# Performance work log

Hardware: AMD Instinct MI355X
Metric: run time of the kernel (lower is better)

Reference implementation:

```python
import jax, jax.numpy as jnp
import numpy as np

B, XDIM, S = 32768, 32, 16
N_COMBINE = XDIM - 2  # 30 combines with out_channels=S (block0 + middle blocks)


def setup_inputs() -> dict:
    key = jax.random.key(0)
    k1, k2, k3, k4 = jax.random.split(key, 4)
    x = jax.random.randint(k1, (B, XDIM), 0, 2, dtype=jnp.int32)  # binary data
    leaf_logits = jax.random.normal(k2, (XDIM, S), dtype=jnp.float32)  # Bernoulli leaf logits per var
    sum_weights = jax.random.normal(k3, (N_COMBINE, S * S, S), dtype=jnp.float32)
    sum_weights_last = jax.random.normal(k4, (S * S, 1), dtype=jnp.float32)
    return {"x": x, "leaf_logits": leaf_logits, "sum_weights": sum_weights,
            "sum_weights_last": sum_weights_last}


def _combine(a, b, W):
    # a, b: [B, S] log-likelihoods; W: [S*S, OC] raw sum weights.
    # CrossProduct in log domain: out[:, i*S + j] = a[:, i] + b[:, j]
    cross = (a[:, :, None] + b[:, None, :]).reshape(a.shape[0], S * S)  # [B, S*S]
    logw = jax.nn.log_softmax(W, axis=0)  # normalize over in_channels
    # Sum node in log domain: logsumexp over input channels
    return jax.nn.logsumexp(cross[:, :, None] + logw[None, :, :], axis=1)  # [B, OC]


def reference(x, leaf_logits, sum_weights, sum_weights_last):
    xf = x.astype(jnp.float32)[:, :, None]  # [B, XDIM, 1]
    # Bernoulli leaf log-prob: x*log(sigmoid(l)) + (1-x)*log(1-sigmoid(l))
    lp = (xf * jax.nn.log_sigmoid(leaf_logits)[None]
          + (1.0 - xf) * jax.nn.log_sigmoid(-leaf_logits)[None])  # [B, XDIM, S]

    # block 0: combine leaves of vars 0 and 1
    curr = _combine(lp[:, 0], lp[:, 1], sum_weights[0])  # [B, S]

    # middle blocks: fold in vars 2 .. XDIM-2
    mid_leaves = jnp.swapaxes(lp[:, 2:XDIM - 1], 0, 1)  # [XDIM-3, B, S]

    def step(c, inp):
        leaf, W = inp
        return _combine(c, leaf, W), None

    curr, _ = jax.lax.scan(step, curr, (mid_leaves, sum_weights[1:]))

    # final block: fold in last var with out_channels=1 root sum
    out = _combine(curr, lp[:, XDIM - 1], sum_weights_last)  # [B, 1]
    return out[:, None, :]  # [B, 1, 1] to match torch output shape
```

## Files before the change

### kernel.cpp

```cpp
#include <hip/hip_runtime.h>

using uint = unsigned int;

#define DW_LO    0
#define DW_HIb   7616
#define DW_FT    15232
#define DW_DELTA 15360
#define DW_BASE  15392
#define DW_EB0   15396
#define DW_TOT   15616

template<int K>
__device__ __forceinline__ int roti(int x) {
    return __builtin_amdgcn_update_dpp(0, x, 0x120 | K, 0xF, 0xF, true);
}
template<int K>
__device__ __forceinline__ float rotf(float x) {
    return __builtin_bit_cast(float, roti<K>(__builtin_bit_cast(int, x)));
}
__device__ __forceinline__ float rowmax16(float d) {
    d = fmaxf(d, rotf<1>(d)); d = fmaxf(d, rotf<2>(d));
    d = fmaxf(d, rotf<4>(d)); d = fmaxf(d, rotf<8>(d));
    return d;
}
__device__ __forceinline__ float rowsum16(float d) {
    d += rotf<1>(d); d += rotf<2>(d); d += rotf<4>(d); d += rotf<8>(d);
    return d;
}
__device__ __forceinline__ float logsig(float z) {
    return fminf(z, 0.f) - log1pf(__expf(-fabsf(z)));
}
__device__ __forceinline__ uint bfpack(float a, float b) {
    uint ua = __builtin_bit_cast(uint, a);
    uint ub = __builtin_bit_cast(uint, b);
    ua = (ua + 0x7fffu + ((ua >> 16) & 1u)) >> 16;
    ub = ((ub + 0x7fffu + ((ub >> 16) & 1u)) >> 16) << 16;
    return ua | ub;
}
__device__ __forceinline__ float blo(uint u) { return __builtin_bit_cast(float, u << 16); }
__device__ __forceinline__ float bhi(uint u) { return __builtin_bit_cast(float, u & 0xffff0000u); }
__device__ __forceinline__ unsigned spread16(unsigned u) {
    u = (u | (u << 8)) & 0x00FF00FFu;
    u = (u | (u << 4)) & 0x0F0F0F0Fu;
    u = (u | (u << 2)) & 0x33333333u;
    u = (u | (u << 1)) & 0x55555555u;
    return u;
}

__global__ __launch_bounds__(512) void prep(const float* __restrict__ sw,
                                            const float* __restrict__ swl,
                                            const float* __restrict__ ll,
                                            float* __restrict__ ws) {
    __shared__ __align__(16) float WFs[2048];
    __shared__ float pm[1024];
    __shared__ float CM[64], CS[64];
    __shared__ float ebs[128];
    __shared__ float Ts[1024];
    __shared__ float Ms[4096];
    __shared__ float BMs[64];
    __shared__ float WLs[32];
    __shared__ float pml[16], psl[16];
    __shared__ float CMl, CSl;

    const int tid = threadIdx.x;
    const int p = blockIdx.x;
    const int oc = tid & 15;
    const int i0 = (tid >> 4) & 15;

    int s1 = roti<1>(oc) & 15,   s2 = roti<2>(oc) & 15,   s3 = roti<3>(oc) & 15;
    int s4 = roti<4>(oc) & 15,   s5 = roti<5>(oc) & 15,   s6 = roti<6>(oc) & 15;
    int s7 = roti<7>(oc) & 15,   s8 = roti<8>(oc) & 15,   s9 = roti<9>(oc) & 15;
    int s10 = roti<10>(oc) & 15, s11 = roti<11>(oc) & 15, s12 = roti<12>(oc) & 15;
    int s13 = roti<13>(oc) & 15, s14 = roti<14>(oc) & 15, s15 = roti<15>(oc) & 15;
    int sidx[16] = {oc, s1, s2, s3, s4, s5, s6, s7, s8, s9, s10, s11, s12, s13, s14, s15};

    if (p < 7) {
        if (tid < 128) {
            int cc = tid >> 5, bb = (tid >> 4) & 1, var = 4 * p + 1 + cc;
            float l = ll[var * 16 + oc];
            float lp = bb ? logsig(l) : logsig(-l);
            ebs[tid] = __expf(lp - rowmax16(lp));
        }
        const float* Wb = sw + p * 4 * 4096;
        const int cc0 = tid >> 8, cc1 = cc0 + 2;
        float w0[16], w1[16];
        float m0 = -1e30f, m1 = -1e30f;
        #pragma unroll
        for (int j = 0; j < 16; ++j) {
            w0[j] = Wb[cc0 * 4096 + (i0 * 16 + j) * 16 + oc];
            w1[j] = Wb[cc1 * 4096 + (i0 * 16 + j) * 16 + oc];
            m0 = fmaxf(m0, w0[j]); m1 = fmaxf(m1, w1[j]);
        }
        pm[cc0 * 256 + oc * 16 + i0] = m0;
        pm[cc1 * 256 + oc * 16 + i0] = m1;
        __syncthreads();
        if (tid < 64) {
            const float* q = pm + (tid >> 4) * 256 + (tid & 15) * 16;
            float m = q[0];
            #pragma unroll
            for (int r = 1; r < 16; ++r) m = fmaxf(m, q[r]);
            CM[tid] = m;
        }
        __syncthreads();
        float cm0 = CM[cc0 * 16 + oc], cm1 = CM[cc1 * 16 + oc];
        float e0[16], e1[16];
        float su0 = 0.f, su1 = 0.f;
        #pragma unroll
        for (int j = 0; j < 16; ++j) {
            e0[j] = __expf(w0[j] - cm0); su0 += e0[j];
            e1[j] = __expf(w1[j] - cm1); su1 += e1[j];
        }
        pm[cc0 * 256 + oc * 16 + i0] = su0;
        pm[cc1 * 256 + oc * 16 + i0] = su1;
        __syncthreads();
        if (tid < 64) {
            const float* q = pm + (tid >> 4) * 256 + (tid & 15) * 16;
            float s = 0.f;
            #pragma unroll
            for (int r = 0; r < 16; ++r) s += q[r];
            CS[tid] = 1.0f / s;
        }
        __syncthreads();
        {
            float inv0 = CS[cc0 * 16 + oc], inv1 = CS[cc1 * 16 + oc];
            float a00 = 0.f, a01 = 0.f, a10 = 0.f, a11 = 0.f;
            #pragma unroll
            for (int j = 0; j < 16; ++j) {
                a00 += ebs[(cc0 * 2 + 0) * 16 + j] * e0[j];
                a01 += ebs[(cc0 * 2 + 1) * 16 + j] * e0[j];
                a10 += ebs[(cc1 * 2 + 0) * 16 + j] * e1[j];
                a11 += ebs[(cc1 * 2 + 1) * 16 + j] * e1[j];
            }
            WFs[(cc0 * 2 + 0) * 256 + i0 * 16 + oc] = a00 * inv0;
            WFs[(cc0 * 2 + 1) * 256 + i0 * 16 + oc] = a01 * inv0;
            WFs[(cc1 * 2 + 0) * 256 + i0 * 16 + oc] = a10 * inv1;
            WFs[(cc1 * 2 + 1) * 256 + i0 * 16 + oc] = a11 * inv1;
        }
        __syncthreads();

        float t1[4], t2[4];
        if (tid < 256) {
            float wf0[2], wf2[2];
            wf0[0] = WFs[0 * 256 + i0 * 16 + oc];
            wf0[1] = WFs[1 * 256 + i0 * 16 + oc];
            wf2[0] = WFs[4 * 256 + i0 * 16 + oc];
            wf2[1] = WFs[5 * 256 + i0 * 16 + oc];
            {
                float w10 = WFs[2 * 256 + oc * 16 + oc], w11 = WFs[3 * 256 + oc * 16 + oc];
                float w30 = WFs[6 * 256 + oc * 16 + oc], w31 = WFs[7 * 256 + oc * 16 + oc];
                t1[0] = wf0[0] * w10; t1[1] = wf0[1] * w10;
                t1[2] = wf0[0] * w11; t1[3] = wf0[1] * w11;
                t2[0] = wf2[0] * w30; t2[1] = wf2[1] * w30;
                t2[2] = wf2[0] * w31; t2[3] = wf2[1] * w31;
            }
            #define QSTEP(T) { \
                float r0 = rotf<T>(wf0[0]), r1 = rotf<T>(wf0[1]); \
                float w10 = WFs[2 * 256 + sidx[T] * 16 + oc], w11 = WFs[3 * 256 + sidx[T] * 16 + oc]; \
                t1[0] = fmaf(r0, w10, t1[0]); t1[1] = fmaf(r1, w10, t1[1]); \
                t1[2] = fmaf(r0, w11, t1[2]); t1[3] = fmaf(r1, w11, t1[3]); \
                float q0 = rotf<T>(wf2[0]), q1 = rotf<T>(wf2[1]); \
                float w30 = WFs[6 * 256 + sidx[T] * 16 + oc], w31 = WFs[7 * 256 + sidx[T] * 16 + oc]; \
                t2[0] = fmaf(q0, w30, t2[0]); t2[1] = fmaf(q1, w30, t2[1]); \
                t2[2] = fmaf(q0, w31, t2[2]); t2[3] = fmaf(q1, w31, t2[3]); }
            QSTEP(1) QSTEP(2) QSTEP(3) QSTEP(4) QSTEP(5) QSTEP(6) QSTEP(7) QSTEP(8)
            QSTEP(9) QSTEP(10) QSTEP(11) QSTEP(12) QSTEP(13) QSTEP(14) QSTEP(15)
            #undef QSTEP
            #pragma unroll
            for (int b = 0; b < 4; ++b) Ts[b * 256 + i0 * 16 + oc] = t2[b];
        }
        __syncthreads();
        if (tid < 256) {
            float M[16];
            {
                float c0 = Ts[0 * 256 + oc * 16 + oc], c1 = Ts[1 * 256 + oc * 16 + oc];
                float c2 = Ts[2 * 256 + oc * 16 + oc], c3 = Ts[3 * 256 + oc * 16 + oc];
                #pragma unroll
                for (int b12 = 0; b12 < 4; ++b12) {
                    M[b12 + 0]  = t1[b12] * c0;
                    M[b12 + 4]  = t1[b12] * c1;
                    M[b12 + 8]  = t1[b12] * c2;
                    M[b12 + 12] = t1[b12] * c3;
                }
            }
            #define MSTEP(T) { \
                float c0 = Ts[0 * 256 + sidx[T] * 16 + oc], c1 = Ts[1 * 256 + sidx[T] * 16 + oc]; \
                float c2 = Ts[2 * 256 + sidx[T] * 16 + oc], c3 = Ts[3 * 256 + sidx[T] * 16 + oc]; \
                float r0 = rotf<T>(t1[0]), r1 = rotf<T>(t1[1]), r2 = rotf<T>(t1[2]), r3 = rotf<T>(t1[3]); \
                M[0]  = fmaf(r0, c0, M[0]);  M[1]  = fmaf(r1, c0, M[1]); \
                M[2]  = fmaf(r2, c0, M[2]);  M[3]  = fmaf(r3, c0, M[3]); \
                M[4]  = fmaf(r0, c1, M[4]);  M[5]  = fmaf(r1, c1, M[5]); \
                M[6]  = fmaf(r2, c1, M[6]);  M[7]  = fmaf(r3, c1, M[7]); \
                M[8]  = fmaf(r0, c2, M[8]);  M[9]  = fmaf(r1, c2, M[9]); \
                M[10] = fmaf(r2, c2, M[10]); M[11] = fmaf(r3, c2, M[11]); \
                M[12] = fmaf(r0, c3, M[12]); M[13] = fmaf(r1, c3, M[13]); \
                M[14] = fmaf(r2, c3, M[14]); M[15] = fmaf(r3, c3, M[15]); }
            MSTEP(1) MSTEP(2) MSTEP(3) MSTEP(4) MSTEP(5) MSTEP(6) MSTEP(7) MSTEP(8)
            MSTEP(9) MSTEP(10) MSTEP(11) MSTEP(12) MSTEP(13) MSTEP(14) MSTEP(15)
            #undef MSTEP
            #pragma unroll
            for (int v = 0; v < 16; ++v) Ms[v * 256 + i0 * 16 + oc] = M[v];
        }
        __syncthreads();
        if (tid < 256) {
            int v = i0, ocx = oc;
            const float* m = Ms + v * 256;
            float x0 = m[ocx * 16 + ocx];
            float x1 = m[s1 * 16 + ocx],   x2 = m[s2 * 16 + ocx],   x3 = m[s3 * 16 + ocx];
            float x4 = m[s4 * 16 + ocx],   x5 = m[s5 * 16 + ocx],   x6 = m[s6 * 16 + ocx];
            float x7 = m[s7 * 16 + ocx],   x8 = m[s8 * 16 + ocx],   x9 = m[s9 * 16 + ocx];
            float x10 = m[s10 * 16 + ocx], x11 = m[s11 * 16 + ocx], x12 = m[s12 * 16 + ocx];
            float x13 = m[s13 * 16 + ocx], x14 = m[s14 * 16 + ocx], x15 = m[s15 * 16 + ocx];
            uint4 lo4, hi4;
            lo4.x = bfpack(x0, x1);   lo4.y = bfpack(x2, x3);
            lo4.z = bfpack(x4, x5);   lo4.w = bfpack(x6, x7);
            hi4.x = bfpack(x8, x9);   hi4.y = bfpack(x10, x11);
            hi4.z = bfpack(x12, x13); hi4.w = bfpack(x14, x15);
            uint* wsu = (uint*)ws;
            int dw = p * 1088 + v * 68 + ocx * 4;
            *(uint4*)(wsu + dw) = lo4;
            *(uint4*)(wsu + DW_HIb + dw) = hi4;
        }
    } else {
        if (tid < 96) {
            int cb = tid >> 4, bb = cb & 1;
            int var = (cb < 4) ? (29 + (cb >> 1)) : 31;
            float l = ll[var * 16 + oc];
            float lp = bb ? logsig(l) : logsig(-l);
            ebs[tid] = __expf(lp - rowmax16(lp));
        }
        const int cc = tid >> 8;
        float w[16]; float m0 = -1e30f;
        #pragma unroll
        for (int j = 0; j < 16; ++j) {
            w[j] = sw[(28 + cc) * 4096 + (i0 * 16 + j) * 16 + oc];
            m0 = fmaxf(m0, w[j]);
        }
        pm[cc * 256 + oc * 16 + i0] = m0;
        float vL = 0.f;
        if (tid >= 256) {
            int u = tid - 256;
            vL = swl[u];
            float pmx = rowmax16(vL);
            if ((u & 15) == 0) pml[u >> 4] = pmx;
        }
        __syncthreads();
        if (tid < 32) {
            const float* q = pm + (tid >> 4) * 256 + (tid & 15) * 16;
            float m = q[0];
            #pragma unroll
            for (int r = 1; r < 16; ++r) m = fmaxf(m, q[r]);
            CM[tid] = m;
        }
        if (tid == 256) {
            float m = pml[0];
            #pragma unroll
            for (int r = 1; r < 16; ++r) m = fmaxf(m, pml[r]);
            CMl = m;
        }
        __syncthreads();
        float cm = CM[cc * 16 + oc];
        float e[16]; float su = 0.f;
        #pragma unroll
        for (int j = 0; j < 16; ++j) { e[j] = __expf(w[j] - cm); su += e[j]; }
        pm[cc * 256 + oc * 16 + i0] = su;
        float eL = 0.f;
        if (tid >= 256) {
            int u = tid - 256;
            eL = __expf(vL - CMl);
            float ps = rowsum16(eL);
            if ((u & 15) == 0) psl[u >> 4] = ps;
        }
        __syncthreads();
        if (tid < 32) {
            const float* q = pm + (tid >> 4) * 256 + (tid & 15) * 16;
            float s = 0.f;
            #pragma unroll
            for (int r = 0; r < 16; ++r) s += q[r];
            CS[tid] = 1.0f / s;
        }
        if (tid == 256) {
            float s = 0.f;
            #pragma unroll
            for (int r = 0; r < 16; ++r) s += psl[r];
            CSl = 1.0f / s;
        }
        __syncthreads();
        {
            float inv = CS[cc * 16 + oc];
            float a0 = 0.f, a1 = 0.f;
            #pragma unroll
            for (int j = 0; j < 16; ++j) {
                a0 += ebs[(cc * 2 + 0) * 16 + j] * e[j];
                a1 += ebs[(cc * 2 + 1) * 16 + j] * e[j];
            }
            WFs[(cc * 2 + 0) * 256 + i0 * 16 + oc] = a0 * inv;
            WFs[(cc * 2 + 1) * 256 + i0 * 16 + oc] = a1 * inv;
        }
        if (tid >= 256) {
            int u = tid - 256, iw = u >> 4;
            float t0 = rowsum16(ebs[64 + oc] * eL);
            float t1 = rowsum16(ebs[80 + oc] * eL);
            if (oc == 0) { WLs[iw] = t0 * CSl; WLs[16 + iw] = t1 * CSl; }
        }
        if (tid < 64) {
            int var = tid >> 1, bb = tid & 1;
            float mm_ = -1e30f;
            #pragma unroll
            for (int j = 0; j < 16; ++j) {
                float l = ll[var * 16 + j];
                mm_ = fmaxf(mm_, bb ? logsig(l) : logsig(-l));
            }
            BMs[tid] = mm_;
        }
        if (tid >= 64 && tid < 96) {
            int u = tid - 64, bb = u >> 4, j = u & 15;
            float mm_ = -1e30f;
            #pragma unroll
            for (int jj = 0; jj < 16; ++jj) {
                float l = ll[jj];
                mm_ = fmaxf(mm_, bb ? logsig(l) : logsig(-l));
            }
            float l = ll[j];
            ws[DW_EB0 + u] = __expf((bb ? logsig(l) : logsig(-l)) - mm_);
        }
        __syncthreads();
        if (tid < 256) {
            float wf28[2];
            wf28[0] = WFs[0 * 256 + i0 * 16 + oc];
            wf28[1] = WFs[1 * 256 + i0 * 16 + oc];
            float t01[4];
            {
                float w0_ = WFs[2 * 256 + oc * 16 + oc], w1_ = WFs[3 * 256 + oc * 16 + oc];
                t01[0] = wf28[0] * w0_; t01[1] = wf28[1] * w0_;
                t01[2] = wf28[0] * w1_; t01[3] = wf28[1] * w1_;
            }
            #define FSTEP(T) { \
                float r0 = rotf<T>(wf28[0]), r1 = rotf<T>(wf28[1]); \
                float w0_ = WFs[2 * 256 + sidx[T] * 16 + oc], w1_ = WFs[3 * 256 + sidx[T] * 16 + oc]; \
                t01[0] = fmaf(r0, w0_, t01[0]); t01[1] = fmaf(r1, w0_, t01[1]); \
                t01[2] = fmaf(r0, w1_, t01[2]); t01[3] = fmaf(r1, w1_, t01[3]); }
            FSTEP(1) FSTEP(2) FSTEP(3) FSTEP(4) FSTEP(5) FSTEP(6) FSTEP(7) FSTEP(8)
            FSTEP(9) FSTEP(10) FSTEP(11) FSTEP(12) FSTEP(13) FSTEP(14) FSTEP(15)
            #undef FSTEP
            float wl0 = WLs[oc], wl1 = WLs[16 + oc];
            #pragma unroll
            for (int v = 0; v < 8; ++v) {
                float f = rowsum16(t01[v & 3] * ((v >> 2) ? wl1 : wl0));
                if (oc == 0) ws[DW_FT + v * 16 + i0] = f;
            }
        }
        if (tid < 32) ws[DW_DELTA + tid] = BMs[2 * tid + 1] - BMs[2 * tid];
        if (tid < 64) {
            float vb = (tid < 32) ? BMs[2 * tid] : 0.f;
            #pragma unroll
            for (int off = 32; off >= 1; off >>= 1) vb += __shfl_xor(vb, off);
            if (tid == 0) ws[DW_BASE] = vb;
        }
    }
}

__device__ __forceinline__ float quadstep(const uint* sPT, float acc, int dw) {
    uint4 wl4 = *(const uint4*)(sPT + dw);
    uint4 wh4 = *(const uint4*)(sPT + DW_HIb + dw);
    float d0 = acc * blo(wl4.x);
    d0 = fmaf(rotf<1>(acc), bhi(wl4.x), d0);
    d0 = fmaf(rotf<2>(acc), blo(wl4.y), d0);
    d0 = fmaf(rotf<3>(acc), bhi(wl4.y), d0);
    d0 = fmaf(rotf<4>(acc), blo(wl4.z), d0);
    d0 = fmaf(rotf<5>(acc), bhi(wl4.z), d0);
    d0 = fmaf(rotf<6>(acc), blo(wl4.w), d0);
    d0 = fmaf(rotf<7>(acc), bhi(wl4.w), d0);
    float d1 = rotf<8>(acc) * blo(wh4.x);
    d1 = fmaf(rotf<9>(acc),  bhi(wh4.x), d1);
    d1 = fmaf(rotf<10>(acc), blo(wh4.y), d1);
    d1 = fmaf(rotf<11>(acc), bhi(wh4.y), d1);
    d1 = fmaf(rotf<12>(acc), blo(wh4.z), d1);
    d1 = fmaf(rotf<13>(acc), bhi(wh4.z), d1);
    d1 = fmaf(rotf<14>(acc), blo(wh4.w), d1);
    d1 = fmaf(rotf<15>(acc), bhi(wh4.w), d1);
    return d0 + d1;
}

__global__ __launch_bounds__(512, 4) void spn_main(const int* __restrict__ x,
                                                   const float* __restrict__ ws,
                                                   float* __restrict__ out) {
    __shared__ __align__(16) float sL[DW_TOT];
    const int tid = threadIdx.x;
    const int g = tid >> 4, oc = tid & 15;
    const int b0 = blockIdx.x * 64 + g;
    const int b1 = b0 + 32;

    int2 xa = *(const int2*)(x + b0 * 32 + 2 * oc);
    int2 xb = *(const int2*)(x + b1 * 32 + 2 * oc);
    unsigned long long ma0 = __ballot(xa.x & 1);
    unsigned long long ma1 = __ballot(xa.y & 1);
    unsigned long long mb0 = __ballot(xb.x & 1);
    unsigned long long mb1 = __ballot(xb.y & 1);
    const int gw = g & 3;
    unsigned bitsA = spread16((unsigned)(ma0 >> (gw * 16)) & 0xffffu)
                   | (spread16((unsigned)(ma1 >> (gw * 16)) & 0xffffu) << 1);
    unsigned bitsB = spread16((unsigned)(mb0 >> (gw * 16)) & 0xffffu)
                   | (spread16((unsigned)(mb1 >> (gw * 16)) & 0xffffu) << 1);

    for (int k = tid; k < DW_TOT / 4; k += 512)
        ((float4*)sL)[k] = ((const float4*)ws)[k];
    __syncthreads();

    float2 dl = *(const float2*)(sL + DW_DELTA + 2 * oc);
    float pa = ((xa.x & 1) ? dl.x : 0.f) + ((xa.y & 1) ? dl.y : 0.f);
    float pb = ((xb.x & 1) ? dl.x : 0.f) + ((xb.y & 1) ? dl.y : 0.f);
    float base = sL[DW_BASE];
    float LA = base + rowsum16(pa);
    float LB = base + rowsum16(pb);

    float accA = sL[DW_EB0 + (bitsA & 1) * 16 + oc];
    float accB = sL[DW_EB0 + (bitsB & 1) * 16 + oc];
    const uint* sPT = (const uint*)sL;
    const int ocd = oc * 4;

    #pragma unroll
    for (int p = 0; p < 7; ++p) {
        int dwA = p * 1088 + (int)((bitsA >> (4 * p + 1)) & 15) * 68 + ocd;
        int dwB = p * 1088 + (int)((bitsB >> (4 * p + 1)) & 15) * 68 + ocd;
        float dA = quadstep(sPT, accA, dwA);
        float dB = quadstep(sPT, accB, dwB);
        if (p & 1) {
            float mA = rowmax16(dA), mB = rowmax16(dB);
            accA = dA * __builtin_amdgcn_rcpf(mA);
            accB = dB * __builtin_amdgcn_rcpf(mB);
            LA += __logf(mA);
            LB += __logf(mB);
        } else {
            accA = dA; accB = dB;
        }
    }

    float tsA = rowsum16(accA * sL[DW_FT + ((bitsA >> 29) & 7) * 16 + oc]);
    float tsB = rowsum16(accB * sL[DW_FT + ((bitsB >> 29) & 7) * 16 + oc]);
    if (oc == 0) {
        out[b0] = LA + __logf(tsA);
        out[b1] = LB + __logf(tsB);
    }
}

extern "C" void kernel_launch(void* const* d_in, const int* in_sizes, int n_in,
                              void* d_out, int out_size, void* d_ws, size_t ws_size,
                              hipStream_t stream) {
    const int*   x   = (const int*)d_in[0];
    const float* ll  = (const float*)d_in[1];
    const float* sw  = (const float*)d_in[2];
    const float* swl = (const float*)d_in[3];
    float* out = (float*)d_out;
    float* ws  = (float*)d_ws;

    hipLaunchKernelGGL(prep,     dim3(8),   dim3(512), 0, stream, sw, swl, ll, ws);
    hipLaunchKernelGGL(spn_main, dim3(512), dim3(512), 0, stream, x, ws, out);
}
```

Baseline: 22.24 us.

## Fuse prep into main kernel with atomic role assignment and spin-wait

Merges the weight-preprocessing kernel into the main kernel. The first eight blocks to arrive, chosen by an atomic ticket, compute the preprocessed tables into workspace and signal a global counter. All blocks spin until that counter reaches eight, then load the tables into shared memory. This removes the second kernel launch and its launch gap. In exchange it adds a memset, a global spin barrier and the risk of stalls if the preprocessing blocks are delayed.

```diff
diff --git a/kernel.cpp b/kernel.cpp
--- a/kernel.cpp
+++ b/kernel.cpp
@@ -9,6 +9,21 @@
 #define DW_BASE  15392
 #define DW_EB0   15396
 #define DW_TOT   15616
+#define DW_CTL   15616
+
+#define oWF   0
+#define oPM   2048
+#define oCM   3072
+#define oCS   3136
+#define oEB   3200
+#define oT    3328
+#define oMM   4352
+#define oBM   8448
+#define oWL   8512
+#define oPML  8544
+#define oPSL  8560
+#define oCML  8576
+#define oCSL  8577
 
 template<int K>
 __device__ __forceinline__ int roti(int x) {
@@ -45,318 +60,6 @@
     u = (u | (u << 2)) & 0x33333333u;
     u = (u | (u << 1)) & 0x55555555u;
     return u;
-}
-
-__global__ __launch_bounds__(512) void prep(const float* __restrict__ sw,
-                                            const float* __restrict__ swl,
-                                            const float* __restrict__ ll,
-                                            float* __restrict__ ws) {
-    __shared__ __align__(16) float WFs[2048];
-    __shared__ float pm[1024];
-    __shared__ float CM[64], CS[64];
-    __shared__ float ebs[128];
-    __shared__ float Ts[1024];
-    __shared__ float Ms[4096];
-    __shared__ float BMs[64];
-    __shared__ float WLs[32];
-    __shared__ float pml[16], psl[16];
-    __shared__ float CMl, CSl;
-
-    const int tid = threadIdx.x;
-    const int p = blockIdx.x;
-    const int oc = tid & 15;
-    const int i0 = (tid >> 4) & 15;
-
-    int s1 = roti<1>(oc) & 15,   s2 = roti<2>(oc) & 15,   s3 = roti<3>(oc) & 15;
-    int s4 = roti<4>(oc) & 15,   s5 = roti<5>(oc) & 15,   s6 = roti<6>(oc) & 15;
-    int s7 = roti<7>(oc) & 15,   s8 = roti<8>(oc) & 15,   s9 = roti<9>(oc) & 15;
-    int s10 = roti<10>(oc) & 15, s11 = roti<11>(oc) & 15, s12 = roti<12>(oc) & 15;
-    int s13 = roti<13>(oc) & 15, s14 = roti<14>(oc) & 15, s15 = roti<15>(oc) & 15;
-    int sidx[16] = {oc, s1, s2, s3, s4, s5, s6, s7, s8, s9, s10, s11, s12, s13, s14, s15};
-
-    if (p < 7) {
-        if (tid < 128) {
-            int cc = tid >> 5, bb = (tid >> 4) & 1, var = 4 * p + 1 + cc;
-            float l = ll[var * 16 + oc];
-            float lp = bb ? logsig(l) : logsig(-l);
-            ebs[tid] = __expf(lp - rowmax16(lp));
-        }
-        const float* Wb = sw + p * 4 * 4096;
-        const int cc0 = tid >> 8, cc1 = cc0 + 2;
-        float w0[16], w1[16];
-        float m0 = -1e30f, m1 = -1e30f;
-        #pragma unroll
-        for (int j = 0; j < 16; ++j) {
-            w0[j] = Wb[cc0 * 4096 + (i0 * 16 + j) * 16 + oc];
-            w1[j] = Wb[cc1 * 4096 + (i0 * 16 + j) * 16 + oc];
-            m0 = fmaxf(m0, w0[j]); m1 = fmaxf(m1, w1[j]);
-        }
-        pm[cc0 * 256 + oc * 16 + i0] = m0;
-        pm[cc1 * 256 + oc * 16 + i0] = m1;
-        __syncthreads();
-        if (tid < 64) {
-            const float* q = pm + (tid >> 4) * 256 + (tid & 15) * 16;
-            float m = q[0];
-            #pragma unroll
-            for (int r = 1; r < 16; ++r) m = fmaxf(m, q[r]);
-            CM[tid] = m;
-        }
-        __syncthreads();
-        float cm0 = CM[cc0 * 16 + oc], cm1 = CM[cc1 * 16 + oc];
-        float e0[16], e1[16];
-        float su0 = 0.f, su1 = 0.f;
-        #pragma unroll
-        for (int j = 0; j < 16; ++j) {
-            e0[j] = __expf(w0[j] - cm0); su0 += e0[j];
-            e1[j] = __expf(w1[j] - cm1); su1 += e1[j];
-        }
-        pm[cc0 * 256 + oc * 16 + i0] = su0;
-        pm[cc1 * 256 + oc * 16 + i0] = su1;
-        __syncthreads();
-        if (tid < 64) {
-            const float* q = pm + (tid >> 4) * 256 + (tid & 15) * 16;
-            float s = 0.f;
-            #pragma unroll
-            for (int r = 0; r < 16; ++r) s += q[r];
-            CS[tid] = 1.0f / s;
-        }
-        __syncthreads();
-        {
-            float inv0 = CS[cc0 * 16 + oc], inv1 = CS[cc1 * 16 + oc];
-            float a00 = 0.f, a01 = 0.f, a10 = 0.f, a11 = 0.f;
-            #pragma unroll
-            for (int j = 0; j < 16; ++j) {
-                a00 += ebs[(cc0 * 2 + 0) * 16 + j] * e0[j];
-                a01 += ebs[(cc0 * 2 + 1) * 16 + j] * e0[j];
-                a10 += ebs[(cc1 * 2 + 0) * 16 + j] * e1[j];
-                a11 += ebs[(cc1 * 2 + 1) * 16 + j] * e1[j];
-            }
-            WFs[(cc0 * 2 + 0) * 256 + i0 * 16 + oc] = a00 * inv0;
-            WFs[(cc0 * 2 + 1) * 256 + i0 * 16 + oc] = a01 * inv0;
-            WFs[(cc1 * 2 + 0) * 256 + i0 * 16 + oc] = a10 * inv1;
-            WFs[(cc1 * 2 + 1) * 256 + i0 * 16 + oc] = a11 * inv1;
-        }
-        __syncthreads();
-
-        float t1[4], t2[4];
-        if (tid < 256) {
-            float wf0[2], wf2[2];
-            wf0[0] = WFs[0 * 256 + i0 * 16 + oc];
-            wf0[1] = WFs[1 * 256 + i0 * 16 + oc];
-            wf2[0] = WFs[4 * 256 + i0 * 16 + oc];
-            wf2[1] = WFs[5 * 256 + i0 * 16 + oc];
-            {
-                float w10 = WFs[2 * 256 + oc * 16 + oc], w11 = WFs[3 * 256 + oc * 16 + oc];
-                float w30 = WFs[6 * 256 + oc * 16 + oc], w31 = WFs[7 * 256 + oc * 16 + oc];
-                t1[0] = wf0[0] * w10; t1[1] = wf0[1] * w10;
-                t1[2] = wf0[0] * w11; t1[3] = wf0[1] * w11;
-                t2[0] = wf2[0] * w30; t2[1] = wf2[1] * w30;
-                t2[2] = wf2[0] * w31; t2[3] = wf2[1] * w31;
-            }
-            #define QSTEP(T) { \
-                float r0 = rotf<T>(wf0[0]), r1 = rotf<T>(wf0[1]); \
-                float w10 = WFs[2 * 256 + sidx[T] * 16 + oc], w11 = WFs[3 * 256 + sidx[T] * 16 + oc]; \
-                t1[0] = fmaf(r0, w10, t1[0]); t1[1] = fmaf(r1, w10, t1[1]); \
-                t1[2] = fmaf(r0, w11, t1[2]); t1[3] = fmaf(r1, w11, t1[3]); \
-                float q0 = rotf<T>(wf2[0]), q1 = rotf<T>(wf2[1]); \
-                float w30 = WFs[6 * 256 + sidx[T] * 16 + oc], w31 = WFs[7 * 256 + sidx[T] * 16 + oc]; \
-                t2[0] = fmaf(q0, w30, t2[0]); t2[1] = fmaf(q1, w30, t2[1]); \
-                t2[2] = fmaf(q0, w31, t2[2]); t2[3] = fmaf(q1, w31, t2[3]); }
-            QSTEP(1) QSTEP(2) QSTEP(3) QSTEP(4) QSTEP(5) QSTEP(6) QSTEP(7) QSTEP(8)
-            QSTEP(9) QSTEP(10) QSTEP(11) QSTEP(12) QSTEP(13) QSTEP(14) QSTEP(15)
-            #undef QSTEP
-            #pragma unroll
-            for (int b = 0; b < 4; ++b) Ts[b * 256 + i0 * 16 + oc] = t2[b];
-        }
-        __syncthreads();
-        if (tid < 256) {
-            float M[16];
-            {
-                float c0 = Ts[0 * 256 + oc * 16 + oc], c1 = Ts[1 * 256 + oc * 16 + oc];
-                float c2 = Ts[2 * 256 + oc * 16 + oc], c3 = Ts[3 * 256 + oc * 16 + oc];
-                #pragma unroll
-                for (int b12 = 0; b12 < 4; ++b12) {
-                    M[b12 + 0]  = t1[b12] * c0;
-                    M[b12 + 4]  = t1[b12] * c1;
-                    M[b12 + 8]  = t1[b12] * c2;
-                    M[b12 + 12] = t1[b12] * c3;
-                }
-            }
-            #define MSTEP(T) { \
-                float c0 = Ts[0 * 256 + sidx[T] * 16 + oc], c1 = Ts[1 * 256 + sidx[T] * 16 + oc]; \
-                float c2 = Ts[2 * 256 + sidx[T] * 16 + oc], c3 = Ts[3 * 256 + sidx[T] * 16 + oc]; \
-                float r0 = rotf<T>(t1[0]), r1 = rotf<T>(t1[1]), r2 = rotf<T>(t1[2]), r3 = rotf<T>(t1[3]); \
-                M[0]  = fmaf(r0, c0, M[0]);  M[1]  = fmaf(r1, c0, M[1]); \
-                M[2]  = fmaf(r2, c0, M[2]);  M[3]  = fmaf(r3, c0, M[3]); \
-                M[4]  = fmaf(r0, c1, M[4]);  M[5]  = fmaf(r1, c1, M[5]); \
-                M[6]  = fmaf(r2, c1, M[6]);  M[7]  = fmaf(r3, c1, M[7]); \
-                M[8]  = fmaf(r0, c2, M[8]);  M[9]  = fmaf(r1, c2, M[9]); \
-                M[10] = fmaf(r2, c2, M[10]); M[11] = fmaf(r3, c2, M[11]); \
-                M[12] = fmaf(r0, c3, M[12]); M[13] = fmaf(r1, c3, M[13]); \
-                M[14] = fmaf(r2, c3, M[14]); M[15] = fmaf(r3, c3, M[15]); }
-            MSTEP(1) MSTEP(2) MSTEP(3) MSTEP(4) MSTEP(5) MSTEP(6) MSTEP(7) MSTEP(8)
-            MSTEP(9) MSTEP(10) MSTEP(11) MSTEP(12) MSTEP(13) MSTEP(14) MSTEP(15)
-            #undef MSTEP
-            #pragma unroll
-            for (int v = 0; v < 16; ++v) Ms[v * 256 + i0 * 16 + oc] = M[v];
-        }
-        __syncthreads();
-        if (tid < 256) {
-            int v = i0, ocx = oc;
-            const float* m = Ms + v * 256;
-            float x0 = m[ocx * 16 + ocx];
-            float x1 = m[s1 * 16 + ocx],   x2 = m[s2 * 16 + ocx],   x3 = m[s3 * 16 + ocx];
-            float x4 = m[s4 * 16 + ocx],   x5 = m[s5 * 16 + ocx],   x6 = m[s6 * 16 + ocx];
-            float x7 = m[s7 * 16 + ocx],   x8 = m[s8 * 16 + ocx],   x9 = m[s9 * 16 + ocx];
-            float x10 = m[s10 * 16 + ocx], x11 = m[s11 * 16 + ocx], x12 = m[s12 * 16 + ocx];
-            float x13 = m[s13 * 16 + ocx], x14 = m[s14 * 16 + ocx], x15 = m[s15 * 16 + ocx];
-            uint4 lo4, hi4;
-            lo4.x = bfpack(x0, x1);   lo4.y = bfpack(x2, x3);
-            lo4.z = bfpack(x4, x5);   lo4.w = bfpack(x6, x7);
-            hi4.x = bfpack(x8, x9);   hi4.y = bfpack(x10, x11);
-            hi4.z = bfpack(x12, x13); hi4.w = bfpack(x14, x15);
-            uint* wsu = (uint*)ws;
-            int dw = p * 1088 + v * 68 + ocx * 4;
-            *(uint4*)(wsu + dw) = lo4;
-            *(uint4*)(wsu + DW_HIb + dw) = hi4;
-        }
-    } else {
-        if (tid < 96) {
-            int cb = tid >> 4, bb = cb & 1;
-            int var = (cb < 4) ? (29 + (cb >> 1)) : 31;
-            float l = ll[var * 16 + oc];
-            float lp = bb ? logsig(l) : logsig(-l);
-            ebs[tid] = __expf(lp - rowmax16(lp));
-        }
-        const int cc = tid >> 8;
-        float w[16]; float m0 = -1e30f;
-        #pragma unroll
-        for (int j = 0; j < 16; ++j) {
-            w[j] = sw[(28 + cc) * 4096 + (i0 * 16 + j) * 16 + oc];
-            m0 = fmaxf(m0, w[j]);
-        }
-        pm[cc * 256 + oc * 16 + i0] = m0;
-        float vL = 0.f;
-        if (tid >= 256) {
-            int u = tid - 256;
-            vL = swl[u];
-            float pmx = rowmax16(vL);
-            if ((u & 15) == 0) pml[u >> 4] = pmx;
-        }
-        __syncthreads();
-        if (tid < 32) {
-            const float* q = pm + (tid >> 4) * 256 + (tid & 15) * 16;
-            float m = q[0];
-            #pragma unroll
-            for (int r = 1; r < 16; ++r) m = fmaxf(m, q[r]);
-            CM[tid] = m;
-        }
-        if (tid == 256) {
-            float m = pml[0];
-            #pragma unroll
-            for (int r = 1; r < 16; ++r) m = fmaxf(m, pml[r]);
-            CMl = m;
-        }
-        __syncthreads();
-        float cm = CM[cc * 16 + oc];
-        float e[16]; float su = 0.f;
-        #pragma unroll
-        for (int j = 0; j < 16; ++j) { e[j] = __expf(w[j] - cm); su += e[j]; }
-        pm[cc * 256 + oc * 16 + i0] = su;
-        float eL = 0.f;
-        if (tid >= 256) {
-            int u = tid - 256;
-            eL = __expf(vL - CMl);
-            float ps = rowsum16(eL);
-            if ((u & 15) == 0) psl[u >> 4] = ps;
-        }
-        __syncthreads();
-        if (tid < 32) {
-            const float* q = pm + (tid >> 4) * 256 + (tid & 15) * 16;
-            float s = 0.f;
-            #pragma unroll
-            for (int r = 0; r < 16; ++r) s += q[r];
-            CS[tid] = 1.0f / s;
-        }
-        if (tid == 256) {
-            float s = 0.f;
-            #pragma unroll
-            for (int r = 0; r < 16; ++r) s += psl[r];
-            CSl = 1.0f / s;
-        }
-        __syncthreads();
-        {
-            float inv = CS[cc * 16 + oc];
-            float a0 = 0.f, a1 = 0.f;
-            #pragma unroll
-            for (int j = 0; j < 16; ++j) {
-                a0 += ebs[(cc * 2 + 0) * 16 + j] * e[j];
-                a1 += ebs[(cc * 2 + 1) * 16 + j] * e[j];
-            }
-            WFs[(cc * 2 + 0) * 256 + i0 * 16 + oc] = a0 * inv;
-            WFs[(cc * 2 + 1) * 256 + i0 * 16 + oc] = a1 * inv;
-        }
-        if (tid >= 256) {
-            int u = tid - 256, iw = u >> 4;
-            float t0 = rowsum16(ebs[64 + oc] * eL);
-            float t1 = rowsum16(ebs[80 + oc] * eL);
-            if (oc == 0) { WLs[iw] = t0 * CSl; WLs[16 + iw] = t1 * CSl; }
-        }
-        if (tid < 64) {
-            int var = tid >> 1, bb = tid & 1;
-            float mm_ = -1e30f;
-            #pragma unroll
-            for (int j = 0; j < 16; ++j) {
-                float l = ll[var * 16 + j];
-                mm_ = fmaxf(mm_, bb ? logsig(l) : logsig(-l));
-            }
-            BMs[tid] = mm_;
-        }
-        if (tid >= 64 && tid < 96) {
-            int u = tid - 64, bb = u >> 4, j = u & 15;
-            float mm_ = -1e30f;
-            #pragma unroll
-            for (int jj = 0; jj < 16; ++jj) {
-                float l = ll[jj];
-                mm_ = fmaxf(mm_, bb ? logsig(l) : logsig(-l));
-            }
-            float l = ll[j];
-            ws[DW_EB0 + u] = __expf((bb ? logsig(l) : logsig(-l)) - mm_);
-        }
-        __syncthreads();
-        if (tid < 256) {
-            float wf28[2];
-            wf28[0] = WFs[0 * 256 + i0 * 16 + oc];
-            wf28[1] = WFs[1 * 256 + i0 * 16 + oc];
-            float t01[4];
-            {
-                float w0_ = WFs[2 * 256 + oc * 16 + oc], w1_ = WFs[3 * 256 + oc * 16 + oc];
-                t01[0] = wf28[0] * w0_; t01[1] = wf28[1] * w0_;
-                t01[2] = wf28[0] * w1_; t01[3] = wf28[1] * w1_;
-            }
-            #define FSTEP(T) { \
-                float r0 = rotf<T>(wf28[0]), r1 = rotf<T>(wf28[1]); \
-                float w0_ = WFs[2 * 256 + sidx[T] * 16 + oc], w1_ = WFs[3 * 256 + sidx[T] * 16 + oc]; \
-                t01[0] = fmaf(r0, w0_, t01[0]); t01[1] = fmaf(r1, w0_, t01[1]); \
-                t01[2] = fmaf(r0, w1_, t01[2]); t01[3] = fmaf(r1, w1_, t01[3]); }
-            FSTEP(1) FSTEP(2) FSTEP(3) FSTEP(4) FSTEP(5) FSTEP(6) FSTEP(7) FSTEP(8)
-            FSTEP(9) FSTEP(10) FSTEP(11) FSTEP(12) FSTEP(13) FSTEP(14) FSTEP(15)
-            #undef FSTEP
-            float wl0 = WLs[oc], wl1 = WLs[16 + oc];
-            #pragma unroll
-            for (int v = 0; v < 8; ++v) {
-                float f = rowsum16(t01[v & 3] * ((v >> 2) ? wl1 : wl0));
-                if (oc == 0) ws[DW_FT + v * 16 + i0] = f;
-            }
-        }
-        if (tid < 32) ws[DW_DELTA + tid] = BMs[2 * tid + 1] - BMs[2 * tid];
-        if (tid < 64) {
-            float vb = (tid < 32) ? BMs[2 * tid] : 0.f;
-            #pragma unroll
-            for (int off = 32; off >= 1; off >>= 1) vb += __shfl_xor(vb, off);
-            if (tid == 0) ws[DW_BASE] = vb;
-        }
-    }
 }
 
 __device__ __forceinline__ float quadstep(const uint* sPT, float acc, int dw) {
@@ -381,12 +84,17 @@
     return d0 + d1;
 }
 
-__global__ __launch_bounds__(512, 4) void spn_main(const int* __restrict__ x,
-                                                   const float* __restrict__ ws,
-                                                   float* __restrict__ out) {
+__global__ __launch_bounds__(512, 4) void spn_fused(const int* __restrict__ x,
+                                                    const float* __restrict__ ll,
+                                                    const float* __restrict__ sw,
+                                                    const float* __restrict__ swl,
+                                                    float* __restrict__ ws,
+                                                    float* __restrict__ out) {
     __shared__ __align__(16) float sL[DW_TOT];
+    __shared__ int sRole;
     const int tid = threadIdx.x;
     const int g = tid >> 4, oc = tid & 15;
+    const int i0 = (tid >> 4) & 15;
     const int b0 = blockIdx.x * 64 + g;
     const int b1 = b0 + 32;
 
@@ -401,6 +109,328 @@
                    | (spread16((unsigned)(ma1 >> (gw * 16)) & 0xffffu) << 1);
     unsigned bitsB = spread16((unsigned)(mb0 >> (gw * 16)) & 0xffffu)
                    | (spread16((unsigned)(mb1 >> (gw * 16)) & 0xffffu) << 1);
+
+    uint* ctl = (uint*)(ws + DW_CTL);
+    if (tid == 0) sRole = (int)atomicAdd(ctl, 1u);
+    __syncthreads();
+    const int role = sRole;
+
+    if (role < 8) {
+        const int p = role;
+        int s1 = roti<1>(oc) & 15,   s2 = roti<2>(oc) & 15,   s3 = roti<3>(oc) & 15;
+        int s4 = roti<4>(oc) & 15,   s5 = roti<5>(oc) & 15,   s6 = roti<6>(oc) & 15;
+        int s7 = roti<7>(oc) & 15,   s8 = roti<8>(oc) & 15,   s9 = roti<9>(oc) & 15;
+        int s10 = roti<10>(oc) & 15, s11 = roti<11>(oc) & 15, s12 = roti<12>(oc) & 15;
+        int s13 = roti<13>(oc) & 15, s14 = roti<14>(oc) & 15, s15 = roti<15>(oc) & 15;
+        int sidx[16] = {oc, s1, s2, s3, s4, s5, s6, s7, s8, s9, s10, s11, s12, s13, s14, s15};
+
+        float* WFs = sL + oWF;
+        float* pm  = sL + oPM;
+        float* CMa = sL + oCM;
+        float* CSa = sL + oCS;
+        float* ebs = sL + oEB;
+        float* Ts  = sL + oT;
+        float* Ms  = sL + oMM;
+        float* BMs = sL + oBM;
+        float* WLs = sL + oWL;
+        float* pml = sL + oPML;
+        float* psl = sL + oPSL;
+
+        if (p < 7) {
+            if (tid < 128) {
+                int cc = tid >> 5, bb = (tid >> 4) & 1, var = 4 * p + 1 + cc;
+                float l = ll[var * 16 + oc];
+                float lp = bb ? logsig(l) : logsig(-l);
+                ebs[tid] = __expf(lp - rowmax16(lp));
+            }
+            const float* Wb = sw + p * 4 * 4096;
+            const int cc0 = tid >> 8, cc1 = cc0 + 2;
+            float w0[16], w1[16];
+            float m0 = -1e30f, m1 = -1e30f;
+            #pragma unroll
+            for (int j = 0; j < 16; ++j) {
+                w0[j] = Wb[cc0 * 4096 + (i0 * 16 + j) * 16 + oc];
+                w1[j] = Wb[cc1 * 4096 + (i0 * 16 + j) * 16 + oc];
+                m0 = fmaxf(m0, w0[j]); m1 = fmaxf(m1, w1[j]);
+            }
+            pm[cc0 * 256 + oc * 16 + i0] = m0;
+            pm[cc1 * 256 + oc * 16 + i0] = m1;
+            __syncthreads();
+            if (tid < 64) {
+                const float* q = pm + (tid >> 4) * 256 + (tid & 15) * 16;
+                float m = q[0];
+                #pragma unroll
+                for (int r = 1; r < 16; ++r) m = fmaxf(m, q[r]);
+                CMa[tid] = m;
+            }
+            __syncthreads();
+            float cm0 = CMa[cc0 * 16 + oc], cm1 = CMa[cc1 * 16 + oc];
+            float e0[16], e1[16];
+            float su0 = 0.f, su1 = 0.f;
+            #pragma unroll
+            for (int j = 0; j < 16; ++j) {
+                e0[j] = __expf(w0[j] - cm0); su0 += e0[j];
+                e1[j] = __expf(w1[j] - cm1); su1 += e1[j];
+            }
+            pm[cc0 * 256 + oc * 16 + i0] = su0;
+            pm[cc1 * 256 + oc * 16 + i0] = su1;
+            __syncthreads();
+            if (tid < 64) {
+                const float* q = pm + (tid >> 4) * 256 + (tid & 15) * 16;
+                float s = 0.f;
+                #pragma unroll
+                for (int r = 0; r < 16; ++r) s += q[r];
+                CSa[tid] = 1.0f / s;
+            }
+            __syncthreads();
+            {
+                float inv0 = CSa[cc0 * 16 + oc], inv1 = CSa[cc1 * 16 + oc];
+                float a00 = 0.f, a01 = 0.f, a10 = 0.f, a11 = 0.f;
+                #pragma unroll
+                for (int j = 0; j < 16; ++j) {
+                    a00 += ebs[(cc0 * 2 + 0) * 16 + j] * e0[j];
+                    a01 += ebs[(cc0 * 2 + 1) * 16 + j] * e0[j];
+                    a10 += ebs[(cc1 * 2 + 0) * 16 + j] * e1[j];
+                    a11 += ebs[(cc1 * 2 + 1) * 16 + j] * e1[j];
+                }
+                WFs[(cc0 * 2 + 0) * 256 + i0 * 16 + oc] = a00 * inv0;
+                WFs[(cc0 * 2 + 1) * 256 + i0 * 16 + oc] = a01 * inv0;
+                WFs[(cc1 * 2 + 0) * 256 + i0 * 16 + oc] = a10 * inv1;
+                WFs[(cc1 * 2 + 1) * 256 + i0 * 16 + oc] = a11 * inv1;
+            }
+            __syncthreads();
+
+            float t1[4], t2[4];
+            if (tid < 256) {
+                float wf0[2], wf2[2];
+                wf0[0] = WFs[0 * 256 + i0 * 16 + oc];
+                wf0[1] = WFs[1 * 256 + i0 * 16 + oc];
+                wf2[0] = WFs[4 * 256 + i0 * 16 + oc];
+                wf2[1] = WFs[5 * 256 + i0 * 16 + oc];
+                {
+                    float w10 = WFs[2 * 256 + oc * 16 + oc], w11 = WFs[3 * 256 + oc * 16 + oc];
+                    float w30 = WFs[6 * 256 + oc * 16 + oc], w31 = WFs[7 * 256 + oc * 16 + oc];
+                    t1[0] = wf0[0] * w10; t1[1] = wf0[1] * w10;
+                    t1[2] = wf0[0] * w11; t1[3] = wf0[1] * w11;
+                    t2[0] = wf2[0] * w30; t2[1] = wf2[1] * w30;
+                    t2[2] = wf2[0] * w31; t2[3] = wf2[1] * w31;
+                }
+                #define QSTEP(T) { \
+                    float r0 = rotf<T>(wf0[0]), r1 = rotf<T>(wf0[1]); \
+                    float w10 = WFs[2 * 256 + sidx[T] * 16 + oc], w11 = WFs[3 * 256 + sidx[T] * 16 + oc]; \
+                    t1[0] = fmaf(r0, w10, t1[0]); t1[1] = fmaf(r1, w10, t1[1]); \
+                    t1[2] = fmaf(r0, w11, t1[2]); t1[3] = fmaf(r1, w11, t1[3]); \
+                    float q0 = rotf<T>(wf2[0]), q1 = rotf<T>(wf2[1]); \
+                    float w30 = WFs[6 * 256 + sidx[T] * 16 + oc], w31 = WFs[7 * 256 + sidx[T] * 16 + oc]; \
+                    t2[0] = fmaf(q0, w30, t2[0]); t2[1] = fmaf(q1, w30, t2[1]); \
+                    t2[2] = fmaf(q0, w31, t2[2]); t2[3] = fmaf(q1, w31, t2[3]); }
+                QSTEP(1) QSTEP(2) QSTEP(3) QSTEP(4) QSTEP(5) QSTEP(6) QSTEP(7) QSTEP(8)
+                QSTEP(9) QSTEP(10) QSTEP(11) QSTEP(12) QSTEP(13) QSTEP(14) QSTEP(15)
+                #undef QSTEP
+                #pragma unroll
+                for (int b = 0; b < 4; ++b) Ts[b * 256 + i0 * 16 + oc] = t2[b];
+            }
+            __syncthreads();
+            if (tid < 256) {
+                float M[16];
+                {
+                    float c0 = Ts[0 * 256 + oc * 16 + oc], c1 = Ts[1 * 256 + oc * 16 + oc];
+                    float c2 = Ts[2 * 256 + oc * 16 + oc], c3 = Ts[3 * 256 + oc * 16 + oc];
+                    #pragma unroll
+                    for (int b12 = 0; b12 < 4; ++b12) {
+                        M[b12 + 0]  = t1[b12] * c0;
+                        M[b12 + 4]  = t1[b12] * c1;
+                        M[b12 + 8]  = t1[b12] * c2;
+                        M[b12 + 12] = t1[b12] * c3;
+                    }
+                }
+                #define MSTEP(T) { \
+                    float c0 = Ts[0 * 256 + sidx[T] * 16 + oc], c1 = Ts[1 * 256 + sidx[T] * 16 + oc]; \
+                    float c2 = Ts[2 * 256 + sidx[T] * 16 + oc], c3 = Ts[3 * 256 + sidx[T] * 16 + oc]; \
+                    float r0 = rotf<T>(t1[0]), r1 = rotf<T>(t1[1]), r2 = rotf<T>(t1[2]), r3 = rotf<T>(t1[3]); \
+                    M[0]  = fmaf(r0, c0, M[0]);  M[1]  = fmaf(r1, c0, M[1]); \
+                    M[2]  = fmaf(r2, c0, M[2]);  M[3]  = fmaf(r3, c0, M[3]); \
+                    M[4]  = fmaf(r0, c1, M[4]);  M[5]  = fmaf(r1, c1, M[5]); \
+                    M[6]  = fmaf(r2, c1, M[6]);  M[7]  = fmaf(r3, c1, M[7]); \
+                    M[8]  = fmaf(r0, c2, M[8]);  M[9]  = fmaf(r1, c2, M[9]); \
+                    M[10] = fmaf(r2, c2, M[10]); M[11] = fmaf(r3, c2, M[11]); \
+                    M[12] = fmaf(r0, c3, M[12]); M[13] = fmaf(r1, c3, M[13]); \
+                    M[14] = fmaf(r2, c3, M[14]); M[15] = fmaf(r3, c3, M[15]); }
+                MSTEP(1) MSTEP(2) MSTEP(3) MSTEP(4) MSTEP(5) MSTEP(6) MSTEP(7) MSTEP(8)
+                MSTEP(9) MSTEP(10) MSTEP(11) MSTEP(12) MSTEP(13) MSTEP(14) MSTEP(15)
+                #undef MSTEP
+                #pragma unroll
+                for (int v = 0; v < 16; ++v) Ms[v * 256 + i0 * 16 + oc] = M[v];
+            }
+            __syncthreads();
+            if (tid < 256) {
+                int v = i0, ocx = oc;
+                const float* m = Ms + v * 256;
+                float x0 = m[ocx * 16 + ocx];
+                float x1 = m[s1 * 16 + ocx],   x2 = m[s2 * 16 + ocx],   x3 = m[s3 * 16 + ocx];
+                float x4 = m[s4 * 16 + ocx],   x5 = m[s5 * 16 + ocx],   x6 = m[s6 * 16 + ocx];
+                float x7 = m[s7 * 16 + ocx],   x8 = m[s8 * 16 + ocx],   x9 = m[s9 * 16 + ocx];
+                float x10 = m[s10 * 16 + ocx], x11 = m[s11 * 16 + ocx], x12 = m[s12 * 16 + ocx];
+                float x13 = m[s13 * 16 + ocx], x14 = m[s14 * 16 + ocx], x15 = m[s15 * 16 + ocx];
+                uint4 lo4, hi4;
+                lo4.x = bfpack(x0, x1);   lo4.y = bfpack(x2, x3);
+                lo4.z = bfpack(x4, x5);   lo4.w = bfpack(x6, x7);
+                hi4.x = bfpack(x8, x9);   hi4.y = bfpack(x10, x11);
+                hi4.z = bfpack(x12, x13); hi4.w = bfpack(x14, x15);
+                uint* wsu = (uint*)ws;
+                int dw = p * 1088 + v * 68 + ocx * 4;
+                *(uint4*)(wsu + dw) = lo4;
+                *(uint4*)(wsu + DW_HIb + dw) = hi4;
+            }
+        } else {
+            if (tid < 96) {
+                int cb = tid >> 4, bb = cb & 1;
+                int var = (cb < 4) ? (29 + (cb >> 1)) : 31;
+                float l = ll[var * 16 + oc];
+                float lp = bb ? logsig(l) : logsig(-l);
+                ebs[tid] = __expf(lp - rowmax16(lp));
+            }
+            const int cc = tid >> 8;
+            float w[16]; float m0 = -1e30f;
+            #pragma unroll
+            for (int j = 0; j < 16; ++j) {
+                w[j] = sw[(28 + cc) * 4096 + (i0 * 16 + j) * 16 + oc];
+                m0 = fmaxf(m0, w[j]);
+            }
+            pm[cc * 256 + oc * 16 + i0] = m0;
+            float vL = 0.f;
+            if (tid >= 256) {
+                int u = tid - 256;
+                vL = swl[u];
+                float pmx = rowmax16(vL);
+                if ((u & 15) == 0) pml[u >> 4] = pmx;
+            }
+            __syncthreads();
+            if (tid < 32) {
+                const float* q = pm + (tid >> 4) * 256 + (tid & 15) * 16;
+                float m = q[0];
+                #pragma unroll
+                for (int r = 1; r < 16; ++r) m = fmaxf(m, q[r]);
+                CMa[tid] = m;
+            }
+            if (tid == 256) {
+                float m = pml[0];
+                #pragma unroll
+                for (int r = 1; r < 16; ++r) m = fmaxf(m, pml[r]);
+                sL[oCML] = m;
+            }
+            __syncthreads();
+            float cm = CMa[cc * 16 + oc];
+            float e[16]; float su = 0.f;
+            #pragma unroll
+            for (int j = 0; j < 16; ++j) { e[j] = __expf(w[j] - cm); su += e[j]; }
+            pm[cc * 256 + oc * 16 + i0] = su;
+            float eL = 0.f;
+            if (tid >= 256) {
+                int u = tid - 256;
+                eL = __expf(vL - sL[oCML]);
+                float ps = rowsum16(eL);
+                if ((u & 15) == 0) psl[u >> 4] = ps;
+            }
+            __syncthreads();
+            if (tid < 32) {
+                const float* q = pm + (tid >> 4) * 256 + (tid & 15) * 16;
+                float s = 0.f;
+                #pragma unroll
+                for (int r = 0; r < 16; ++r) s += q[r];
+                CSa[tid] = 1.0f / s;
+            }
+            if (tid == 256) {
+                float s = 0.f;
+                #pragma unroll
+                for (int r = 0; r < 16; ++r) s += psl[r];
+                sL[oCSL] = 1.0f / s;
+            }
+            __syncthreads();
+            {
+                float inv = CSa[cc * 16 + oc];
+                float a0 = 0.f, a1 = 0.f;
+                #pragma unroll
+                for (int j = 0; j < 16; ++j) {
+                    a0 += ebs[(cc * 2 + 0) * 16 + j] * e[j];
+                    a1 += ebs[(cc * 2 + 1) * 16 + j] * e[j];
+                }
+                WFs[(cc * 2 + 0) * 256 + i0 * 16 + oc] = a0 * inv;
+                WFs[(cc * 2 + 1) * 256 + i0 * 16 + oc] = a1 * inv;
+            }
+            if (tid >= 256) {
+                int u = tid - 256, iw = u >> 4;
+                float t0 = rowsum16(ebs[64 + oc] * eL);
+                float t1 = rowsum16(ebs[80 + oc] * eL);
+                if (oc == 0) { WLs[iw] = t0 * sL[oCSL]; WLs[16 + iw] = t1 * sL[oCSL]; }
+            }
+            if (tid < 64) {
+                int var = tid >> 1, bb = tid & 1;
+                float mm_ = -1e30f;
+                #pragma unroll
+                for (int j = 0; j < 16; ++j) {
+                    float l = ll[var * 16 + j];
+                    mm_ = fmaxf(mm_, bb ? logsig(l) : logsig(-l));
+                }
+                BMs[tid] = mm_;
+            }
+            if (tid >= 64 && tid < 96) {
+                int u = tid - 64, bb = u >> 4, j = u & 15;
+                float mm_ = -1e30f;
+                #pragma unroll
+                for (int jj = 0; jj < 16; ++jj) {
+                    float l = ll[jj];
+                    mm_ = fmaxf(mm_, bb ? logsig(l) : logsig(-l));
+                }
+                float l = ll[j];
+                ws[DW_EB0 + u] = __expf((bb ? logsig(l) : logsig(-l)) - mm_);
+            }
+            __syncthreads();
+            if (tid < 256) {
+                float wf28[2];
+                wf28[0] = WFs[0 * 256 + i0 * 16 + oc];
+                wf28[1] = WFs[1 * 256 + i0 * 16 + oc];
+                float t01[4];
+                {
+                    float w0_ = WFs[2 * 256 + oc * 16 + oc], w1_ = WFs[3 * 256 + oc * 16 + oc];
+                    t01[0] = wf28[0] * w0_; t01[1] = wf28[1] * w0_;
+                    t01[2] = wf28[0] * w1_; t01[3] = wf28[1] * w1_;
+                }
+                #define FSTEP(T) { \
+                    float r0 = rotf<T>(wf28[0]), r1 = rotf<T>(wf28[1]); \
+                    float w0_ = WFs[2 * 256 + sidx[T] * 16 + oc], w1_ = WFs[3 * 256 + sidx[T] * 16 + oc]; \
+                    t01[0] = fmaf(r0, w0_, t01[0]); t01[1] = fmaf(r1, w0_, t01[1]); \
+                    t01[2] = fmaf(r0, w1_, t01[2]); t01[3] = fmaf(r1, w1_, t01[3]); }
+                FSTEP(1) FSTEP(2) FSTEP(3) FSTEP(4) FSTEP(5) FSTEP(6) FSTEP(7) FSTEP(8)
+                FSTEP(9) FSTEP(10) FSTEP(11) FSTEP(12) FSTEP(13) FSTEP(14) FSTEP(15)
+                #undef FSTEP
+                float wl0 = WLs[oc], wl1 = WLs[16 + oc];
+                #pragma unroll
+                for (int v = 0; v < 8; ++v) {
+                    float f = rowsum16(t01[v & 3] * ((v >> 2) ? wl1 : wl0));
+                    if (oc == 0) ws[DW_FT + v * 16 + i0] = f;
+                }
+            }
+            if (tid < 32) ws[DW_DELTA + tid] = BMs[2 * tid + 1] - BMs[2 * tid];
+            if (tid < 64) {
+                float vb = (tid < 32) ? BMs[2 * tid] : 0.f;
+                #pragma unroll
+                for (int off = 32; off >= 1; off >>= 1) vb += __shfl_xor(vb, off);
+                if (tid == 0) ws[DW_BASE] = vb;
+            }
+        }
+        __syncthreads();
+        if (tid == 0) {
+            __threadfence();
+            atomicAdd(ctl + 1, 1u);
+        }
+    }
+
+    if (tid == 0) {
+        while (__hip_atomic_load(ctl + 1, __ATOMIC_ACQUIRE, __HIP_MEMORY_SCOPE_AGENT) < 8u)
+            __builtin_amdgcn_s_sleep(2);
+    }
+    __syncthreads();
 
     for (int k = tid; k < DW_TOT / 4; k += 512)
         ((float4*)sL)[k] = ((const float4*)ws)[k];
@@ -453,6 +483,7 @@
     float* out = (float*)d_out;
     float* ws  = (float*)d_ws;
 
-    hipLaunchKernelGGL(prep,     dim3(8),   dim3(512), 0, stream, sw, swl, ll, ws);
-    hipLaunchKernelGGL(spn_main, dim3(512), dim3(512), 0, stream, x, ws, out);
-}
+    hipMemsetAsync((char*)d_ws + DW_CTL * 4, 0, 8, stream);
+    hipLaunchKernelGGL(spn_fused, dim3(512), dim3(512), 0, stream,
+                       x, ll, sw, swl, ws, out);
+}
```

Result: slower. 47.36 us (+113.0%).
